# Kernel optimization log

Measured on AMD Instinct MI355X. Metric: run time of the kernel, lower is better.

Reference implementation:

```python
import jax, jax.numpy as jnp
import numpy as np

BATCH = 32768
NJETS = 10
NCOMBOS = 22
FF = 200
NSEL = 6
EPS = 1e-5
METRIC = jnp.array([1.0, -1.0, -1.0, -1.0], dtype=jnp.float32)  # (E,px,py,pz) Minkowski


def _cola(v, w_combo):
    # v: [b, n, 4]; w_combo: [c, n] -> [b, n+c, 4] (identity rows + learned combos)
    combos = jnp.einsum('cj,bjv->bcv', w_combo, v)
    return jnp.concatenate([v, combos], axis=1)


def _lola(v, w_e, w_d):
    # v: [b, n, 4] -> [b, n, 5] features: m2, pT, E, w_e.E, w_d.d2
    m2 = jnp.einsum('biv,v,biv->bi', v, METRIC, v)           # invariant mass^2
    pt = jnp.sqrt(v[..., 1] ** 2 + v[..., 2] ** 2)           # transverse momentum
    E = v[..., 0]
    we = jnp.einsum('ij,bj->bi', w_e, E)
    # pairwise Minkowski distances via gram trick (avoids [b,n,n,4] tensor)
    gram = jnp.einsum('biv,v,bjv->bij', v, METRIC, v)        # [b, n, n]
    d2 = m2[:, :, None] + m2[:, None, :] - 2.0 * gram
    wd = jnp.einsum('ij,bij->bi', w_d, d2)
    return jnp.stack([m2, pt, E, we, wd], axis=-1)


def _batchnorm(x, gamma, beta):
    # torch BatchNorm1d in train mode: per-feature batch mean / biased var
    mu = jnp.mean(x, axis=0)
    var = jnp.mean((x - mu) ** 2, axis=0)
    return (x - mu) * jax.lax.rsqrt(var + EPS) * gamma + beta


def _head(v, cola_w, w_e, w_d, bn_g, bn_b, w1, b1, w2, b2):
    x = _cola(v, cola_w)
    f = _lola(x, w_e, w_d).reshape(x.shape[0], -1)  # [b, ntotal*5]
    f = _batchnorm(f, bn_g, bn_b)
    h = jax.nn.relu(f @ w1.T + b1)
    return h @ w2.T + b2


def setup_inputs() -> dict:
    key = jax.random.key(0)
    ks = jax.random.split(key, 20)
    n_isr = NJETS + NCOMBOS   # 32
    n_dec = NSEL + NCOMBOS    # 28
    f_isr, f_dec = n_isr * 5, n_dec * 5
    rn = lambda k, s, sc=0.1: jax.random.normal(k, s, jnp.float32) * sc
    return {
        'vectors': jax.random.normal(ks[0], (BATCH, NJETS, 4), jnp.float32),
        'isr_cola_w': rn(ks[1], (NCOMBOS, NJETS)),
        'isr_we': rn(ks[2], (n_isr, n_isr)),
        'isr_wd': rn(ks[3], (n_isr, n_isr)),
        'isr_bn_g': jnp.ones((f_isr,), jnp.float32),
        'isr_bn_b': jnp.zeros((f_isr,), jnp.float32),
        'isr_w1': rn(ks[4], (FF, f_isr)),
        'isr_b1': jnp.zeros((FF,), jnp.float32),
        'isr_w2': rn(ks[5], (NJETS, FF)),
        'isr_b2': jnp.zeros((NJETS,), jnp.float32),
        'dec_cola_w': rn(ks[6], (NCOMBOS, NSEL)),
        'dec_we': rn(ks[7], (n_dec, n_dec)),
        'dec_wd': rn(ks[8], (n_dec, n_dec)),
        'dec_bn_g': jnp.ones((f_dec,), jnp.float32),
        'dec_bn_b': jnp.zeros((f_dec,), jnp.float32),
        'dec_w1': rn(ks[9], (FF, f_dec)),
        'dec_b1': jnp.zeros((FF,), jnp.float32),
        'dec_w2': rn(ks[10], (11, FF)),
        'dec_b2': jnp.zeros((11,), jnp.float32),
    }


def reference(vectors, isr_cola_w, isr_we, isr_wd, isr_bn_g, isr_bn_b,
              isr_w1, isr_b1, isr_w2, isr_b2,
              dec_cola_w, dec_we, dec_wd, dec_bn_g, dec_bn_b,
              dec_w1, dec_b1, dec_w2, dec_b2):
    out_isr = _head(vectors, isr_cola_w, isr_we, isr_wd, isr_bn_g, isr_bn_b,
                    isr_w1, isr_b1, isr_w2, isr_b2)  # [b, njets]
    # iterative argmin+delete of (njets-6) jets == keep top-6 scores, original order
    scores = jax.lax.stop_gradient(out_isr)  # torch code detaches isrtag
    _, idx = jax.lax.top_k(scores, NSEL)
    idx = jnp.sort(idx, axis=1)  # np.delete preserves original ordering
    selected = jnp.take_along_axis(vectors, idx[:, :, None], axis=1)  # [b, 6, 4]
    out_dec = _head(selected, dec_cola_w, dec_we, dec_wd, dec_bn_g, dec_bn_b,
                    dec_w1, dec_b1, dec_w2, dec_b2)  # [b, 11]
    return jnp.concatenate([out_isr, out_dec], axis=1)  # [b, njets+11]
```

## Files before the change

### kernel.cpp

```cpp
#include <hip/hip_runtime.h>


#define BATCH 32768
#define NJ 10
#define FFDIM 200
#define OUTSTRIDE 21
#define NFEATBLK 4096

typedef float v2f __attribute__((ext_vector_type(2)));

template<int NIN, int NP>
__global__ __launch_bounds__(256) void feat_kernel(
    const float* __restrict__ vin,
    const float* __restrict__ cola,
    const float* __restrict__ we,
    const float* __restrict__ wd,
    float* __restrict__ fout,
    float* __restrict__ psum,
    float* __restrict__ psq)
{
    constexpr int NC = 22;
    constexpr int F  = NP * 5;
    constexpr int RB = 8;
    constexpr int SW = NP + 1;
    constexpr int SF = F + 8;
    __shared__ float s_cola[NC * NIN];
    __shared__ float s_we[NP * SW];
    __shared__ float s_wd[NP * SW];
    __shared__ float4 s_x[RB][NP];
    __shared__ float s_m2[RB][NP];
    __shared__ float s_f[RB * SF];

    const int tid = threadIdx.x;
    const int blk = blockIdx.x;

    for (int k = tid; k < NC * NIN; k += 256) s_cola[k] = cola[k];
    for (int k = tid; k < NP * NP; k += 256) {
        const int i2 = k / NP, j2 = k - i2 * NP;
        s_we[i2 * SW + j2] = we[k];
        s_wd[i2 * SW + j2] = wd[k];
    }
    for (int k = tid; k < RB * NIN * 4; k += 256)
        ((float*)&s_x[0][0])[(k / (NIN * 4)) * NP * 4 + (k % (NIN * 4))] =
            vin[(size_t)blk * RB * NIN * 4 + k];
    __syncthreads();

    const int r = tid >> 5;
    const int i = tid & 31;

    if (i >= NIN && i < NP) {
        const int c = i - NIN;
        float4 x = make_float4(0.f, 0.f, 0.f, 0.f);
        #pragma unroll
        for (int j = 0; j < NIN; j++) {
            const float w = s_cola[c * NIN + j];
            const float4 xj = s_x[r][j];
            x.x += w * xj.x; x.y += w * xj.y; x.z += w * xj.z; x.w += w * xj.w;
        }
        s_x[r][i] = x;
    }
    __syncthreads();

    float m2 = 0.f, pt = 0.f;
    float4 xi = make_float4(0.f, 0.f, 0.f, 0.f);
    if (i < NP) {
        xi = s_x[r][i];
        m2 = xi.x * xi.x - xi.y * xi.y - xi.z * xi.z - xi.w * xi.w;
        pt = sqrtf(xi.y * xi.y + xi.z * xi.z);
        s_m2[r][i] = m2;
    }
    __syncthreads();
    if (i < NP) {
        float wesum = 0.f, wdsum = 0.f;
        for (int j = 0; j < NP; j++) {
            const float4 xj = s_x[r][j];
            wesum += s_we[i * SW + j] * xj.x;
            const float g = xi.x * xj.x - xi.y * xj.y - xi.z * xj.z - xi.w * xj.w;
            wdsum += s_wd[i * SW + j] * (m2 + s_m2[r][j] - 2.0f * g);
        }
        s_f[r * SF + i * 5 + 0] = m2;
        s_f[r * SF + i * 5 + 1] = pt;
        s_f[r * SF + i * 5 + 2] = xi.x;
        s_f[r * SF + i * 5 + 3] = wesum;
        s_f[r * SF + i * 5 + 4] = wdsum;
    }
    __syncthreads();

    for (int q = tid; q < RB * F; q += 256) {
        const int rr = q / F, c = q - rr * F;
        fout[(size_t)blk * RB * F + q] = s_f[rr * SF + c];
    }

    if (tid < F) {
        float s = 0.f, s2 = 0.f;
        #pragma unroll
        for (int rr = 0; rr < RB; rr++) {
            const float v = s_f[rr * SF + tid];
            s += v; s2 += v * v;
        }
        psum[(size_t)tid * NFEATBLK + blk] = s;
        psq [(size_t)tid * NFEATBLK + blk] = s2;
    }
}

template<int F>
__global__ __launch_bounds__(256) void bn_reduce(
    const float* __restrict__ psum, const float* __restrict__ psq,
    const float* __restrict__ gamma, const float* __restrict__ beta,
    float* __restrict__ bn)
{
    __shared__ float s1[256], s2[256];
    const int f = blockIdx.x, tid = threadIdx.x;
    float a = 0.f, b = 0.f;
    for (int bk = tid; bk < NFEATBLK; bk += 256) {
        a += psum[(size_t)f * NFEATBLK + bk];
        b += psq [(size_t)f * NFEATBLK + bk];
    }
    s1[tid] = a; s2[tid] = b; __syncthreads();
    for (int s = 128; s > 0; s >>= 1) {
        if (tid < s) { s1[tid] += s1[tid + s]; s2[tid] += s2[tid + s]; }
        __syncthreads();
    }
    if (tid == 0) {
        const float mu  = s1[0] / (float)BATCH;
        const float var = s2[0] / (float)BATCH - mu * mu;
        const float sc  = gamma[f] * rsqrtf(var + 1e-5f);
        bn[f]     = sc;
        bn[F + f] = beta[f] - mu * sc;
    }
}

template<int G, int NF, int NOUT>
__device__ __forceinline__ void do_group(
    const float* __restrict__ frow,
    const float* __restrict__ w1,
    const float* __restrict__ b1,
    const float* __restrict__ w2,
    int n0,
    v2f* __restrict__ part2)
{
    v2f acc[G];
    #pragma unroll
    for (int j = 0; j < G; j++) acc[j] = (v2f){0.f, 0.f};

    for (int kc = 0; kc < NF / 4; kc++) {
        const float4 fa = *reinterpret_cast<const float4*>(&frow[kc * 4]);
        const v2f f01 = (v2f){fa.x, fa.y}, f23 = (v2f){fa.z, fa.w};
        #pragma unroll
        for (int j = 0; j < G; j++) {
            const float4 wv = *reinterpret_cast<const float4*>(
                w1 + (size_t)(n0 + j) * NF + kc * 4);
            acc[j] += (v2f){wv.x, wv.y} * f01;
            acc[j] += (v2f){wv.z, wv.w} * f23;
        }
    }
    #pragma unroll
    for (int a = 0; a < G / 2; a++) {
        float h0 = acc[2 * a][0] + acc[2 * a][1] + b1[n0 + 2 * a];
        float h1 = acc[2 * a + 1][0] + acc[2 * a + 1][1] + b1[n0 + 2 * a + 1];
        h0 = h0 > 0.f ? h0 : 0.f;
        h1 = h1 > 0.f ? h1 : 0.f;
        const v2f hp = (v2f){h0, h1};
        #pragma unroll
        for (int o = 0; o < NOUT; o++) {
            const v2f w2v = *reinterpret_cast<const v2f*>(
                w2 + (size_t)o * FFDIM + n0 + 2 * a);
            part2[o] += hp * w2v;
        }
    }
}

template<int NF, int NOUT, bool SELECT>
__global__ __launch_bounds__(256, 2) void mlp_kernel(
    const float* __restrict__ fin,
    const float* __restrict__ bn,
    const float* __restrict__ w1,
    const float* __restrict__ b1,
    const float* __restrict__ w2,
    const float* __restrict__ b2,
    const float* __restrict__ vectors,
    float* __restrict__ selout,
    float* __restrict__ out,
    int out_off)
{
    constexpr int RB = 64;
    constexpr int SU = (NF == 160) ? 164 : 148;
    __shared__ __align__(16) float U[RB * SU];
    __shared__ __align__(16) float s_scale[NF], s_shift[NF];
    __shared__ float s_out[RB * 12];
    __shared__ int   s_idx[RB * 6];

    const int tid = threadIdx.x;
    const int blk = blockIdx.x;
    const int w = __builtin_amdgcn_readfirstlane(tid >> 6);
    const int r = tid & 63;

    for (int k = tid; k < NF; k += 256) { s_scale[k] = bn[k]; s_shift[k] = bn[NF + k]; }
    __syncthreads();

    {
        constexpr int NF4 = NF / 4;
        const float4* fb4 = reinterpret_cast<const float4*>(fin + (size_t)blk * RB * NF);
        for (int q4 = tid; q4 < RB * NF4; q4 += 256) {
            const int row = q4 / NF4, c = (q4 - row * NF4) * 4;
            const float4 v = fb4[q4];
            const float4 sc = *reinterpret_cast<const float4*>(&s_scale[c]);
            const float4 sh = *reinterpret_cast<const float4*>(&s_shift[c]);
            float4 o;
            o.x = v.x * sc.x + sh.x; o.y = v.y * sc.y + sh.y;
            o.z = v.z * sc.z + sh.z; o.w = v.w * sc.w + sh.w;
            *reinterpret_cast<float4*>(&U[row * SU + c]) = o;
        }
    }
    __syncthreads();

    const float* frow = &U[r * SU];
    const int n0 = w * 50;
    v2f part2[NOUT];
    #pragma unroll
    for (int o = 0; o < NOUT; o++) part2[o] = (v2f){0.f, 0.f};

    do_group<18, NF, NOUT>(frow, w1, b1, w2, n0,      part2);
    do_group<16, NF, NOUT>(frow, w1, b1, w2, n0 + 18, part2);
    do_group<16, NF, NOUT>(frow, w1, b1, w2, n0 + 34, part2);
    __syncthreads();

    float* s_part = U;
    #pragma unroll
    for (int o = 0; o < NOUT; o++)
        s_part[(w * RB + r) * 12 + o] = part2[o][0] + part2[o][1];
    __syncthreads();

    for (int q = tid; q < RB * NOUT; q += 256) {
        const int row = q / NOUT, o = q - row * NOUT;
        float v = b2[o];
        #pragma unroll
        for (int ww = 0; ww < 4; ww++) v += s_part[(ww * RB + row) * 12 + o];
        s_out[row * 12 + o] = v;
    }
    __syncthreads();

    if (SELECT) {
        if (tid < RB) {
            float sc[10];
            #pragma unroll
            for (int o = 0; o < 10; o++) sc[o] = s_out[tid * 12 + o];
            bool used[10];
            #pragma unroll
            for (int o = 0; o < 10; o++) used[o] = false;
            int ids[6];
            for (int k = 0; k < 6; k++) {
                float m = -3.0e38f; int mi = 0;
                for (int o = 0; o < 10; o++)
                    if (!used[o] && sc[o] > m) { m = sc[o]; mi = o; }
                used[mi] = true; ids[k] = mi;
            }
            for (int a2i = 1; a2i < 6; a2i++) {
                const int v = ids[a2i]; int bp = a2i - 1;
                while (bp >= 0 && ids[bp] > v) { ids[bp + 1] = ids[bp]; bp--; }
                ids[bp + 1] = v;
            }
            #pragma unroll
            for (int k = 0; k < 6; k++) s_idx[tid * 6 + k] = ids[k];
        }
        __syncthreads();
        for (int q = tid; q < RB * 6; q += 256) {
            const int r2 = q / 6, j = q - r2 * 6;
            reinterpret_cast<float4*>(selout)[(size_t)blk * RB * 6 + q] =
                reinterpret_cast<const float4*>(vectors)
                    [(size_t)(blk * RB + r2) * NJ + s_idx[r2 * 6 + j]];
        }
    }

    for (int q = tid; q < RB * NOUT; q += 256) {
        const int r2 = q / NOUT, o = q - r2 * NOUT;
        out[(size_t)(blk * RB + r2) * OUTSTRIDE + out_off + o] = s_out[r2 * 12 + o];
    }
}

extern "C" void kernel_launch(void* const* d_in, const int* in_sizes, int n_in,
                              void* d_out, int out_size, void* d_ws, size_t ws_size,
                              hipStream_t stream) {
    const float* vectors  = (const float*)d_in[0];
    const float* isr_cola = (const float*)d_in[1];
    const float* isr_we   = (const float*)d_in[2];
    const float* isr_wd   = (const float*)d_in[3];
    const float* isr_bn_g = (const float*)d_in[4];
    const float* isr_bn_b = (const float*)d_in[5];
    const float* isr_w1   = (const float*)d_in[6];
    const float* isr_b1   = (const float*)d_in[7];
    const float* isr_w2   = (const float*)d_in[8];
    const float* isr_b2   = (const float*)d_in[9];
    const float* dec_cola = (const float*)d_in[10];
    const float* dec_we   = (const float*)d_in[11];
    const float* dec_wd   = (const float*)d_in[12];
    const float* dec_bn_g = (const float*)d_in[13];
    const float* dec_bn_b = (const float*)d_in[14];
    const float* dec_w1   = (const float*)d_in[15];
    const float* dec_b1   = (const float*)d_in[16];
    const float* dec_w2   = (const float*)d_in[17];
    const float* dec_b2   = (const float*)d_in[18];
    float* out = (float*)d_out;
    float* ws  = (float*)d_ws;

    float* f_buf  = ws;
    float* sel    = f_buf + 5242880;
    float* ps     = sel + 786432;
    float* pq     = ps + 655360;
    float* bn_i   = pq + 655360;
    float* bn_d   = bn_i + 320;

    feat_kernel<10, 32><<<4096, 256, 0, stream>>>(vectors, isr_cola, isr_we, isr_wd,
                                                  f_buf, ps, pq);
    bn_reduce<160><<<160, 256, 0, stream>>>(ps, pq, isr_bn_g, isr_bn_b, bn_i);
    mlp_kernel<160, 10, true><<<512, 256, 0, stream>>>(f_buf, bn_i, isr_w1, isr_b1,
                                                       isr_w2, isr_b2, vectors, sel,
                                                       out, 0);
    feat_kernel<6, 28><<<4096, 256, 0, stream>>>(sel, dec_cola, dec_we, dec_wd,
                                                 f_buf, ps, pq);
    bn_reduce<140><<<140, 256, 0, stream>>>(ps, pq, dec_bn_g, dec_bn_b, bn_d);
    mlp_kernel<140, 11, false><<<512, 256, 0, stream>>>(f_buf, bn_d, dec_w1, dec_b1,
                                                        dec_w2, dec_b2, nullptr, nullptr,
                                                        out, 10);
}
```

Measured before the change: 169.5 us.

## Register-tile the MLP first layer with double-buffered shared-memory W1 staging

The MLP kernel's first layer switches from one-row-per-thread with per-wave scalar W1 loads to an 8x7 register tile per thread (8 rows by 7 hidden units). The W1 column chunks are double-buffered through shared memory and prefetched one step ahead. The hidden activations are then written to shared memory, and a separate second-layer pass lets each wave compute a subset of outputs per row. The aim is more reuse of features and weights from registers and fewer redundant global W1 loads. The cost is a block-wide sync per K-chunk and larger shared-memory and register use.

Result: faster. 156.5 us (-7.7%).

```diff
diff --git a/kernel.cpp b/kernel.cpp
--- a/kernel.cpp
+++ b/kernel.cpp
@@ -130,46 +130,6 @@
     }
 }
 
-template<int G, int NF, int NOUT>
-__device__ __forceinline__ void do_group(
-    const float* __restrict__ frow,
-    const float* __restrict__ w1,
-    const float* __restrict__ b1,
-    const float* __restrict__ w2,
-    int n0,
-    v2f* __restrict__ part2)
-{
-    v2f acc[G];
-    #pragma unroll
-    for (int j = 0; j < G; j++) acc[j] = (v2f){0.f, 0.f};
-
-    for (int kc = 0; kc < NF / 4; kc++) {
-        const float4 fa = *reinterpret_cast<const float4*>(&frow[kc * 4]);
-        const v2f f01 = (v2f){fa.x, fa.y}, f23 = (v2f){fa.z, fa.w};
-        #pragma unroll
-        for (int j = 0; j < G; j++) {
-            const float4 wv = *reinterpret_cast<const float4*>(
-                w1 + (size_t)(n0 + j) * NF + kc * 4);
-            acc[j] += (v2f){wv.x, wv.y} * f01;
-            acc[j] += (v2f){wv.z, wv.w} * f23;
-        }
-    }
-    #pragma unroll
-    for (int a = 0; a < G / 2; a++) {
-        float h0 = acc[2 * a][0] + acc[2 * a][1] + b1[n0 + 2 * a];
-        float h1 = acc[2 * a + 1][0] + acc[2 * a + 1][1] + b1[n0 + 2 * a + 1];
-        h0 = h0 > 0.f ? h0 : 0.f;
-        h1 = h1 > 0.f ? h1 : 0.f;
-        const v2f hp = (v2f){h0, h1};
-        #pragma unroll
-        for (int o = 0; o < NOUT; o++) {
-            const v2f w2v = *reinterpret_cast<const v2f*>(
-                w2 + (size_t)o * FFDIM + n0 + 2 * a);
-            part2[o] += hp * w2v;
-        }
-    }
-}
-
 template<int NF, int NOUT, bool SELECT>
 __global__ __launch_bounds__(256, 2) void mlp_kernel(
     const float* __restrict__ fin,
@@ -183,18 +143,23 @@
     float* __restrict__ out,
     int out_off)
 {
-    constexpr int RB = 64;
-    constexpr int SU = (NF == 160) ? 164 : 148;
-    __shared__ __align__(16) float U[RB * SU];
-    __shared__ __align__(16) float s_scale[NF], s_shift[NF];
+    constexpr int RB  = 64;
+    constexpr int SU  = (NF == 160) ? 164 : 148;
+    constexpr int SH  = 204;
+    constexpr int NCH = NF / 4;
+    __shared__ __align__(16) float UH[RB * SH];
+    __shared__ __align__(16) float s_w[2][224 * 4];
     __shared__ float s_out[RB * 12];
     __shared__ int   s_idx[RB * 6];
 
     const int tid = threadIdx.x;
     const int blk = blockIdx.x;
-    const int w = __builtin_amdgcn_readfirstlane(tid >> 6);
-    const int r = tid & 63;
-
+    float* s_scale = &UH[RB * SU];
+    float* s_shift = s_scale + NF;
+
+    const int wrow = (tid < 200) ? tid : 199;
+    float4 wv;
+    if (tid < 224) wv = *reinterpret_cast<const float4*>(w1 + (size_t)wrow * NF);
     for (int k = tid; k < NF; k += 256) { s_scale[k] = bn[k]; s_shift[k] = bn[NF + k]; }
     __syncthreads();
 
@@ -204,39 +169,94 @@
         for (int q4 = tid; q4 < RB * NF4; q4 += 256) {
             const int row = q4 / NF4, c = (q4 - row * NF4) * 4;
             const float4 v = fb4[q4];
-            const float4 sc = *reinterpret_cast<const float4*>(&s_scale[c]);
-            const float4 sh = *reinterpret_cast<const float4*>(&s_shift[c]);
             float4 o;
-            o.x = v.x * sc.x + sh.x; o.y = v.y * sc.y + sh.y;
-            o.z = v.z * sc.z + sh.z; o.w = v.w * sc.w + sh.w;
-            *reinterpret_cast<float4*>(&U[row * SU + c]) = o;
-        }
-    }
-    __syncthreads();
-
-    const float* frow = &U[r * SU];
-    const int n0 = w * 50;
-    v2f part2[NOUT];
+            o.x = v.x * s_scale[c + 0] + s_shift[c + 0];
+            o.y = v.y * s_scale[c + 1] + s_shift[c + 1];
+            o.z = v.z * s_scale[c + 2] + s_shift[c + 2];
+            o.w = v.w * s_scale[c + 3] + s_shift[c + 3];
+            *reinterpret_cast<float4*>(&UH[row * SU + c]) = o;
+        }
+    }
+    if (tid < 224) {
+        *reinterpret_cast<float4*>(&s_w[0][tid * 4]) = wv;
+        wv = *reinterpret_cast<const float4*>(w1 + (size_t)wrow * NF + 4);
+    }
+    __syncthreads();
+
+    const int rg = tid & 7;
+    const int ng = tid >> 3;
+    v2f acc[7][8];
     #pragma unroll
-    for (int o = 0; o < NOUT; o++) part2[o] = (v2f){0.f, 0.f};
-
-    do_group<18, NF, NOUT>(frow, w1, b1, w2, n0,      part2);
-    do_group<16, NF, NOUT>(frow, w1, b1, w2, n0 + 18, part2);
-    do_group<16, NF, NOUT>(frow, w1, b1, w2, n0 + 34, part2);
-    __syncthreads();
-
-    float* s_part = U;
+    for (int j = 0; j < 7; j++)
+        #pragma unroll
+        for (int i = 0; i < 8; i++) acc[j][i] = (v2f){0.f, 0.f};
+
+    for (int kt = 0; kt < NCH; kt++) {
+        const int b = kt & 1;
+        float4 wq[7], fq[8];
+        #pragma unroll
+        for (int j = 0; j < 7; j++)
+            wq[j] = *reinterpret_cast<const float4*>(&s_w[b][(ng * 7 + j) * 4]);
+        #pragma unroll
+        for (int i = 0; i < 8; i++)
+            fq[i] = *reinterpret_cast<const float4*>(&UH[(rg * 8 + i) * SU + kt * 4]);
+        #pragma unroll
+        for (int j = 0; j < 7; j++) {
+            const v2f wlo = (v2f){wq[j].x, wq[j].y};
+            const v2f whi = (v2f){wq[j].z, wq[j].w};
+            #pragma unroll
+            for (int i = 0; i < 8; i++) {
+                acc[j][i] += wlo * (v2f){fq[i].x, fq[i].y};
+                acc[j][i] += whi * (v2f){fq[i].z, fq[i].w};
+            }
+        }
+        if (tid < 224 && kt + 1 < NCH) {
+            *reinterpret_cast<float4*>(&s_w[b ^ 1][tid * 4]) = wv;
+            const int kn = (kt + 2 < NCH) ? (kt + 2) * 4 : (NCH - 1) * 4;
+            wv = *reinterpret_cast<const float4*>(w1 + (size_t)wrow * NF + kn);
+        }
+        __syncthreads();
+    }
+
     #pragma unroll
-    for (int o = 0; o < NOUT; o++)
-        s_part[(w * RB + r) * 12 + o] = part2[o][0] + part2[o][1];
-    __syncthreads();
-
-    for (int q = tid; q < RB * NOUT; q += 256) {
-        const int row = q / NOUT, o = q - row * NOUT;
-        float v = b2[o];
-        #pragma unroll
-        for (int ww = 0; ww < 4; ww++) v += s_part[(ww * RB + row) * 12 + o];
-        s_out[row * 12 + o] = v;
+    for (int j = 0; j < 7; j++) {
+        const int n = ng * 7 + j;
+        if (n < 200) {
+            const float bb = b1[n];
+            #pragma unroll
+            for (int i = 0; i < 8; i++) {
+                const float h = acc[j][i][0] + acc[j][i][1] + bb;
+                UH[(rg * 8 + i) * SH + n] = h > 0.f ? h : 0.f;
+            }
+        }
+    }
+    __syncthreads();
+
+    const int w = __builtin_amdgcn_readfirstlane(tid >> 6);
+    const int r = tid & 63;
+    {
+        v2f a2[3];
+        #pragma unroll
+        for (int m = 0; m < 3; m++) a2[m] = (v2f){0.f, 0.f};
+        for (int kc = 0; kc < FFDIM / 4; kc++) {
+            const float4 hv = *reinterpret_cast<const float4*>(&UH[r * SH + kc * 4]);
+            const v2f hlo = (v2f){hv.x, hv.y}, hhi = (v2f){hv.z, hv.w};
+            #pragma unroll
+            for (int m = 0; m < 3; m++) {
+                const int o = w + 4 * m;
+                if (o < NOUT) {
+                    const float4 w2v = *reinterpret_cast<const float4*>(
+                        w2 + (size_t)o * FFDIM + kc * 4);
+                    a2[m] += (v2f){w2v.x, w2v.y} * hlo;
+                    a2[m] += (v2f){w2v.z, w2v.w} * hhi;
+                }
+            }
+        }
+        #pragma unroll
+        for (int m = 0; m < 3; m++) {
+            const int o = w + 4 * m;
+            if (o < NOUT) s_out[r * 12 + o] = a2[m][0] + a2[m][1] + b2[o];
+        }
     }
     __syncthreads();
 
```
